# Kernel tuning notes

Hardware: AMD Instinct MI355X
Metric: run time of the kernel (lower is better)

The kernel has to match this reference:

```python
import jax, jax.numpy as jnp
import numpy as np

N = 50000      # nodes
E = 800000     # edges (before self-loops)
G = 500        # graphs
IN = 128       # in_channels
HID = 32       # hidden_channels per head
HEADS = 4
C = HID * HEADS        # 128, per-layer output dim
L = 3                  # num_layers
HL = (L * C) // 2      # 192, JK-LSTM hidden size (PyG convention)
OUT = 2
NEG_SLOPE = 0.2


def setup_inputs() -> dict:
    key = jax.random.key(0)
    ks = iter(jax.random.split(key, 40))
    inp = {}
    inp['x'] = jax.random.normal(next(ks), (N, IN), dtype=jnp.float32)
    inp['edge_index'] = jax.random.randint(next(ks), (2, E), 0, N, dtype=jnp.int32)
    inp['batch'] = jnp.sort(jax.random.randint(next(ks), (N,), 0, G, dtype=jnp.int32))
    s = 0.1
    for i, in_dim in enumerate([IN, C, C]):
        inp[f'W{i}'] = jax.random.normal(next(ks), (in_dim, C), dtype=jnp.float32) * s
        inp[f'as{i}'] = jax.random.normal(next(ks), (HEADS, HID), dtype=jnp.float32) * s
        inp[f'ad{i}'] = jax.random.normal(next(ks), (HEADS, HID), dtype=jnp.float32) * s
        inp[f'b{i}'] = jnp.zeros((C,), dtype=jnp.float32)
    for d in ['f', 'b']:
        inp[f'Wih_{d}'] = jax.random.normal(next(ks), (4 * HL, C), dtype=jnp.float32) * s
        inp[f'Whh_{d}'] = jax.random.normal(next(ks), (4 * HL, HL), dtype=jnp.float32) * s
        inp[f'bih_{d}'] = jnp.zeros((4 * HL,), dtype=jnp.float32)
        inp[f'bhh_{d}'] = jnp.zeros((4 * HL,), dtype=jnp.float32)
    inp['Wa'] = jax.random.normal(next(ks), (2 * HL, 1), dtype=jnp.float32) * s
    inp['ba'] = jnp.zeros((1,), dtype=jnp.float32)
    inp['Wl'] = jax.random.normal(next(ks), (C, OUT), dtype=jnp.float32) * s
    inp['bl'] = jnp.zeros((OUT,), dtype=jnp.float32)
    return inp


def gat_conv(h_in, src, dst, W, a_s, a_d, b, n):
    # h: [n, heads, hid]
    h = (h_in @ W).reshape(n, HEADS, HID)
    es = (h * a_s).sum(-1)   # [n, heads]
    ed = (h * a_d).sum(-1)
    e = jax.nn.leaky_relu(es[src] + ed[dst], NEG_SLOPE)  # [e, heads]
    m = jax.ops.segment_max(e, dst, num_segments=n)
    ex = jnp.exp(e - m[dst])
    ssum = jax.ops.segment_sum(ex, dst, num_segments=n)
    alpha = ex / (ssum[dst] + 1e-16)
    out = jax.ops.segment_sum(h[src] * alpha[:, :, None], dst, num_segments=n)
    return out.reshape(n, HEADS * HID) + b


def lstm_dir(xseq, Wih, Whh, bih, bhh):
    # xseq: [L, n, C] -> hs: [L, n, HL]; torch gate order i,f,g,o
    n = xseq.shape[1]
    h0 = jnp.zeros((n, HL), xseq.dtype)

    def step(carry, xt):
        h, c = carry
        z = xt @ Wih.T + h @ Whh.T + bih + bhh
        i, f, g, o = jnp.split(z, 4, axis=-1)
        c = jax.nn.sigmoid(f) * c + jax.nn.sigmoid(i) * jnp.tanh(g)
        h = jax.nn.sigmoid(o) * jnp.tanh(c)
        return (h, c), h

    _, hs = jax.lax.scan(step, (h0, h0), xseq)
    return hs


def reference(x, edge_index, batch, W0, as0, ad0, b0, W1, as1, ad1, b1,
              W2, as2, ad2, b2, Wih_f, Whh_f, bih_f, bhh_f,
              Wih_b, Whh_b, bih_b, bhh_b, Wa, ba, Wl, bl):
    n = x.shape[0]
    loop = jnp.arange(n, dtype=edge_index.dtype)
    src = jnp.concatenate([edge_index[0], loop])  # add_self_loops=True
    dst = jnp.concatenate([edge_index[1], loop])
    h = x
    xs = []
    for (W, a_s, a_d, b) in [(W0, as0, ad0, b0), (W1, as1, ad1, b1), (W2, as2, ad2, b2)]:
        h = jax.nn.relu(gat_conv(h, src, dst, W, a_s, a_d, b, n))
        xs.append(h)  # dropout is identity in eval mode
    xstack = jnp.stack(xs, axis=1)  # [n, L, C]
    xseq = jnp.stack(xs, axis=0)    # [L, n, C]
    hs_f = lstm_dir(xseq, Wih_f, Whh_f, bih_f, bhh_f)
    hs_b = lstm_dir(xseq[::-1], Wih_b, Whh_b, bih_b, bhh_b)[::-1]
    lo = jnp.concatenate([hs_f, hs_b], axis=-1)       # [L, n, 2*HL]
    score = jnp.einsum('lnh,h->nl', lo, Wa[:, 0]) + ba[0]
    att = jax.nn.softmax(score, axis=-1)              # [n, L]
    jk = jnp.einsum('nlc,nl->nc', xstack, att)        # [n, C]
    ones = jnp.ones((n,), x.dtype)
    counts = jax.ops.segment_sum(ones, batch, num_segments=G)
    pooled = jax.ops.segment_sum(jk, batch, num_segments=G) / jnp.maximum(counts, 1.0)[:, None]
    return pooled @ Wl + bl  # [G, OUT]
```

## Files before the change

### kernel.cpp

```cpp
#include <hip/hip_runtime.h>
#include <math.h>

#define CDIV(a,b) (((a)+(b)-1)/(b))

typedef _Float16 f16;
typedef _Float16 f16x8 __attribute__((ext_vector_type(8)));
typedef float f32x4 __attribute__((ext_vector_type(4)));

__device__ __forceinline__ float rcpf(float x){ return __builtin_amdgcn_rcpf(x); }
__device__ __forceinline__ float fsig(float x){ return rcpf(1.0f+__expf(-x)); }
__device__ __forceinline__ float ftanh(float x){ float e=__expf(2.0f*x); return 1.0f-2.0f*rcpf(e+1.0f); }

__global__ void zero_kernel(float* __restrict__ p, size_t n){
  size_t i=(size_t)blockIdx.x*blockDim.x+threadIdx.x;
  size_t st=(size_t)gridDim.x*blockDim.x;
  for(;i<n;i+=st) p[i]=0.0f;
}

__global__ void f2h_kernel(const float* __restrict__ s, f16* __restrict__ d, size_t n){
  size_t i=(size_t)blockIdx.x*blockDim.x+threadIdx.x;
  size_t st=(size_t)gridDim.x*blockDim.x;
  for(;i<n;i+=st) d[i]=(f16)s[i];
}
__global__ void wtrans_kernel(const float* __restrict__ W, f16* __restrict__ hi,
                              f16* __restrict__ lo){
  int o=blockIdx.x, i=threadIdx.x;
  float f=W[(size_t)i*128+o];
  f16 h=(f16)f; hi[o*128+i]=h; lo[o*128+i]=(f16)(f-(float)h);
}
__global__ void lstm_wprep(const float* __restrict__ W, f16* __restrict__ hi, int ld){
  int rn=blockIdx.x; int k=threadIdx.x;
  int j=rn>>2, gate=rn&3;
  hi[(size_t)rn*ld+k]=(f16)W[(size_t)(gate*192+j)*ld + k];
}
__global__ void lstm_bprep(const float* __restrict__ bih, const float* __restrict__ bhh,
                           float* __restrict__ bI){
  int rn=blockIdx.x*blockDim.x+threadIdx.x;
  if(rn<768){ int j=rn>>2,g=rn&3; int go=g*192+j; bI[rn]=bih[go]+bhh[go]; }
}

__global__ void hist_kernel(const int* __restrict__ ei, int E, int N, int* __restrict__ deg){
  int e=blockIdx.x*blockDim.x+threadIdx.x;
  if(e>=E+N) return;
  int d=(e<E)? ei[E+e] : (e-E);
  atomicAdd(&deg[d],1);
}
__global__ void scan1_kernel(const int* __restrict__ deg, int* __restrict__ offs,
                             int* __restrict__ bsums, int N){
  __shared__ int sd[1024];
  int t=threadIdx.x;
  int i=blockIdx.x*1024+t;
  int v=(i<N)?deg[i]:0;
  sd[t]=v;
  __syncthreads();
  for(int s=1;s<1024;s<<=1){
    int u=(t>=s)?sd[t-s]:0;
    __syncthreads();
    sd[t]+=u;
    __syncthreads();
  }
  if(i<N) offs[i]=sd[t]-v;
  if(t==1023) bsums[blockIdx.x]=sd[1023];
}
__global__ void scan2_kernel(int* __restrict__ bsums, int* __restrict__ offs, int NB, int N){
  if(threadIdx.x==0&&blockIdx.x==0){
    int run=0;
    for(int b=0;b<NB;b++){int s=bsums[b]; bsums[b]=run; run+=s;}
    offs[N]=run;
  }
}
__global__ void scan3_kernel(int* __restrict__ offs, const int* __restrict__ bsums,
                             int* __restrict__ cursor, int N){
  int i=blockIdx.x*blockDim.x+threadIdx.x;
  if(i<N){
    int o=offs[i]+bsums[i>>10];
    offs[i]=o;
    cursor[i]=o;
  }
}
__global__ void scatter_kernel(const int* __restrict__ ei, int E, int N,
                               int* __restrict__ cursor, int* __restrict__ csr){
  int e=blockIdx.x*blockDim.x+threadIdx.x;
  if(e>=E+N) return;
  int s,d;
  if(e<E){ s=ei[e]; d=ei[E+e]; } else { s=e-E; d=s; }
  int pos=atomicAdd(&cursor[d],1);
  csr[pos]=s;
}

__global__ void goffs_kernel(const int* __restrict__ batch, int N, int G,
                             int* __restrict__ goffs){
  int g=blockIdx.x*blockDim.x+threadIdx.x;
  if (g>G) return;
  if (g==G){ goffs[G]=N; return; }
  int lo=0, hi=N;
  while (lo<hi){ int mid=(lo+hi)>>1; if (batch[mid]<g) lo=mid+1; else hi=mid; }
  goffs[g]=lo;
}

struct GemmDesc {
  const f16* aq[2][12];
  const f16* bq[2][12];
  int lda[12], ldb[12];
  int nq, nd, M, GY, NXB;
  f16* htmp; const float* as_; const float* ad_; float* es; float* ed;
  f16* h16[2]; f16* cbuf[2]; const float* bias[2]; const float* wa[2];
  float* score; int l_out[2]; int firstStep; int lastStep;
};

template<int MODE>
__global__ __launch_bounds__(256) void gemm_mfma(GemmDesc d){
  __shared__ __align__(16) char smraw[33792];
  const int TILE = 128*32;
  f16* Ab0=(f16*)smraw;      f16* Ab1=Ab0+TILE;
  f16* Bb0=Ab1+TILE;         f16* Bb1=Bb0+TILE;
  float* EP = (float*)smraw;

  const int wg = blockIdx.x;
  const int xcd = wg & 7, kk0 = wg >> 3;
  const int nxt = d.nd * d.NXB;
  const int xbg = kk0 % nxt;
  const int yp  = xcd + 8*(kk0 / nxt);
  if (yp >= d.GY) return;
  const int dir = (xbg >= d.NXB) ? 1 : 0;
  const int xb  = xbg - dir*d.NXB;

  const int t = threadIdx.x;
  const int wv = t>>6, ln = t&63;
  const int m0 = yp*128, n0 = xb*128;
  const int wr = (wv>>1)*64, wc = (wv&1)*64;
  f32x4 acc[4][4];
#pragma unroll
  for(int i=0;i<4;i++)
#pragma unroll
  for(int j=0;j<4;j++) acc[i][j]=(f32x4){0.f,0.f,0.f,0.f};

  const int gs = ((ln&3) - ((ln>>3)&3)) & 3;
  const int gp = ((ln>>4) + (((ln&15)>>1)&3)) & 3;

  int offA128[2],offA192[2],offB128[2],offB192[2];
#pragma unroll
  for(int i=0;i<2;i++){
    int ga = m0 + i*64 + wv*16 + (ln>>2); if (ga >= d.M) ga = d.M-1;
    int gb = n0 + i*64 + wv*16 + (ln>>2);
    offA128[i]=ga*128+gs*8; offA192[i]=ga*192+gs*8;
    offB128[i]=gb*128+gs*8; offB192[i]=gb*192+gs*8;
  }

  auto issue=[&](int q,int buf){
    const f16* aS=d.aq[dir][q]; const bool wa_=(d.lda[q]==192);
    const f16* bS=d.bq[dir][q]; const bool wb_=(d.ldb[q]==192);
    f16* Adst = buf? Ab1:Ab0;
    f16* Bdst = buf? Bb1:Bb0;
#pragma unroll
    for(int i=0;i<2;i++){
      int offa = wa_? offA192[i]:offA128[i];
      __builtin_amdgcn_global_load_lds(
        (const __attribute__((address_space(1))) unsigned int*)(aS+offa),
        (__attribute__((address_space(3))) unsigned int*)&Adst[(i*64+wv*16)*32],16,0,0);
      int offb = wb_? offB192[i]:offB128[i];
      __builtin_amdgcn_global_load_lds(
        (const __attribute__((address_space(1))) unsigned int*)(bS+offb),
        (__attribute__((address_space(3))) unsigned int*)&Bdst[(i*64+wv*16)*32],16,0,0);
    }
  };

  issue(0,0);
  for (int s=0; s<d.nq; s++){
    const int cur = s&1;
    if (s+1<d.nq){
      issue(s+1,cur^1);
      asm volatile("s_waitcnt vmcnt(4)" ::: "memory");
    } else {
      asm volatile("s_waitcnt vmcnt(0)" ::: "memory");
    }
    __builtin_amdgcn_sched_barrier(0);
    __builtin_amdgcn_s_barrier();
    __builtin_amdgcn_sched_barrier(0);
    const f16* As = cur? Ab1:Ab0;
    const f16* Bs = cur? Bb1:Bb0;
    f16x8 av[4], bv[4];
#pragma unroll
    for (int i=0;i<4;i++)
      av[i] = *(const f16x8*)&As[(wr + i*16 + (ln&15))*32 + gp*8];
#pragma unroll
    for (int j=0;j<4;j++)
      bv[j] = *(const f16x8*)&Bs[(wc + j*16 + (ln&15))*32 + gp*8];
#pragma unroll
    for (int i=0;i<4;i++)
#pragma unroll
    for (int j=0;j<4;j++)
      acc[i][j] = __builtin_amdgcn_mfma_f32_16x16x32_f16(av[i], bv[j], acc[i][j], 0,0,0);
    __builtin_amdgcn_sched_barrier(0);
    __builtin_amdgcn_s_barrier();
  }

  const int lc2 = ln&15, lr4 = (ln>>4)*4;
  const int row4 = t>>2, q4 = t&3;
#pragma unroll
  for (int ph=0; ph<2; ph++){
    __syncthreads();
    if ((wv>>1) == ph){
#pragma unroll
      for (int i=0;i<4;i++){
#pragma unroll
        for (int jf=0;jf<4;jf++){
          int col = wc + jf*16 + lc2;
#pragma unroll
          for (int r=0;r<4;r++)
            EP[(i*16+lr4+r)*132 + col] = acc[i][jf][r];
        }
      }
    }
    __syncthreads();
    int grow = m0 + ph*64 + row4;
    if (grow < d.M){
      if (MODE==0){
        float s=0.f, dd=0.f;
        const float* asp = d.as_ + q4*32;
        const float* adp = d.ad_ + q4*32;
#pragma unroll
        for (int q8=0;q8<4;q8++){
          f16x8 pk;
#pragma unroll
          for (int r=0;r<8;r++){
            float v = EP[row4*132 + q4*32 + q8*8 + r];
            pk[r] = (f16)v;
            s  += v*asp[q8*8+r];
            dd += v*adp[q8*8+r];
          }
          *(f16x8*)&d.htmp[(size_t)grow*128 + q4*32 + q8*8] = pk;
        }
        d.es[grow*4+q4] = s;
        d.ed[grow*4+q4] = dd;
      } else {
        float sc = 0.f;
        int jg0 = xb*32 + q4*8;
        size_t hbase = (size_t)grow*192 + jg0;
        const float* bI = d.bias[dir] + xb*128 + q4*32;
        f16* h16d = d.h16[dir];
        f16* cbufd = d.cbuf[dir];
        const float* wad = d.wa[dir];
        f16x8 cold8;
        if (!d.firstStep) cold8 = *(const f16x8*)&cbufd[hbase];
        f16x8 hl, cl;
#pragma unroll
        for (int j=0;j<8;j++){
          float4 z = *(float4*)&EP[row4*132 + q4*32 + j*4];
          float zi=z.x+bI[j*4+0], zf=z.y+bI[j*4+1], zg=z.z+bI[j*4+2], zo=z.w+bI[j*4+3];
          float cold = d.firstStep ? 0.f : (float)cold8[j];
          float c = fsig(zf)*cold + fsig(zi)*ftanh(zg);
          float h = fsig(zo)*ftanh(c);
          cl[j] = (f16)c;
          hl[j] = (f16)h;
          sc += h * wad[jg0+j];
        }
        if (!d.lastStep){
          *(f16x8*)&cbufd[hbase] = cl;
          *(f16x8*)&h16d[hbase] = hl;
        }
        sc += __shfl_xor(sc,1);
        sc += __shfl_xor(sc,2);
        if (q4==0) atomicAdd(&d.score[(size_t)grow*3 + d.l_out[dir]], sc);
      }
    }
  }
}

__global__ __launch_bounds__(256) void attn_kernel(const f16* __restrict__ htmp,
   const float* __restrict__ es, const float* __restrict__ ed,
   const int* __restrict__ offs, const int* __restrict__ csr,
   const float* __restrict__ bias, f16* __restrict__ xsl, int N){
  int v=blockIdx.x*4+(threadIdx.x>>6);
  if(v>=N) return;
  int lane=threadIdx.x&63;
  int hd=lane>>4;
  int c0=lane*2;
  int beg=offs[v], end=offs[v+1];
  float edv=ed[v*4+hd];
  float ssum=0.f,a0=0.f,a1=0.f;
  int i=beg;
  for(; i+4<=end; i+=4){
    int s0=csr[i],s1=csr[i+1],s2=csr[i+2],s3=csr[i+3];
    float E0=es[s0*4+hd],E1=es[s1*4+hd],E2=es[s2*4+hd],E3=es[s3*4+hd];
    unsigned u0=*(const unsigned*)&htmp[(size_t)s0*128+c0];
    unsigned u1=*(const unsigned*)&htmp[(size_t)s1*128+c0];
    unsigned u2=*(const unsigned*)&htmp[(size_t)s2*128+c0];
    unsigned u3=*(const unsigned*)&htmp[(size_t)s3*128+c0];
    float e0=E0+edv; e0=(e0>0.f)?e0:0.2f*e0; float x0=__expf(e0);
    float e1=E1+edv; e1=(e1>0.f)?e1:0.2f*e1; float x1=__expf(e1);
    float e2=E2+edv; e2=(e2>0.f)?e2:0.2f*e2; float x2=__expf(e2);
    float e3=E3+edv; e3=(e3>0.f)?e3:0.2f*e3; float x3=__expf(e3);
    ssum += (x0+x1)+(x2+x3);
    union {unsigned u; f16 h[2];} p0,p1,p2,p3;
    p0.u=u0; p1.u=u1; p2.u=u2; p3.u=u3;
    a0 += x0*(float)p0.h[0] + x1*(float)p1.h[0] + x2*(float)p2.h[0] + x3*(float)p3.h[0];
    a1 += x0*(float)p0.h[1] + x1*(float)p1.h[1] + x2*(float)p2.h[1] + x3*(float)p3.h[1];
  }
  for(; i<end; i++){
    int s=csr[i];
    float e=es[s*4+hd]+edv;
    e=(e>0.f)?e:0.2f*e;
    float ex=__expf(e);
    ssum+=ex;
    union {unsigned u; f16 h[2];} pk;
    pk.u = *reinterpret_cast<const unsigned*>(&htmp[(size_t)s*128+c0]);
    a0+=ex*(float)pk.h[0]; a1+=ex*(float)pk.h[1];
  }
  float inv=1.0f/(ssum+1e-16f);
  float o0=fmaxf(a0*inv+bias[c0],0.f), o1=fmaxf(a1*inv+bias[c0+1],0.f);
  union { f16 h[2]; unsigned u; } pko;
  pko.h[0]=(f16)o0; pko.h[1]=(f16)o1;
  *reinterpret_cast<unsigned*>(&xsl[(size_t)v*128+c0]) = pko.u;
}

__global__ __launch_bounds__(256) void jk_pool_kernel(const f16* __restrict__ xs, size_t xstride,
   const float* __restrict__ score, const int* __restrict__ goffs,
   float* __restrict__ pooled, int G){
  int g=blockIdx.x;
  int beg=goffs[g], end=goffs[g+1];
  int c=threadIdx.x&127, half=threadIdx.x>>7;
  float acc=0.f;
  for(int n=beg+half; n<end; n+=2){
    float s0=score[n*3],s1=score[n*3+1],s2=score[n*3+2];
    float m=fmaxf(s0,fmaxf(s1,s2));
    float e0=__expf(s0-m),e1=__expf(s1-m),e2=__expf(s2-m);
    float inv=rcpf(e0+e1+e2);
    size_t base=(size_t)n*128+c;
    acc += ((float)xs[base]*e0+(float)xs[xstride+base]*e1+(float)xs[2*xstride+base]*e2)*inv;
  }
  __shared__ float red[128];
  if(half==1) red[c]=acc;
  __syncthreads();
  if(half==0){
    float tot=acc+red[c];
    float cnt=(float)(end-beg);
    pooled[(size_t)g*128+c]=tot*rcpf(fmaxf(cnt,1.0f));
  }
}

__global__ __launch_bounds__(128) void final_kernel(const float* __restrict__ pooled,
   const float* __restrict__ Wl, const float* __restrict__ bl,
   float* __restrict__ out, int G){
  int g=blockIdx.x; int c=threadIdx.x;
  float pv=pooled[(size_t)g*128+c];
  float p0=pv*Wl[c*2], p1=pv*Wl[c*2+1];
  for(int s=32;s>=1;s>>=1){ p0+=__shfl_down(p0,s); p1+=__shfl_down(p1,s); }
  __shared__ float sm[4];
  int w=c>>6;
  if((c&63)==0){ sm[w*2]=p0; sm[w*2+1]=p1; }
  __syncthreads();
  if(c==0){
    out[g*2+0]=sm[0]+sm[2]+bl[0];
    out[g*2+1]=sm[1]+sm[3]+bl[1];
  }
}

extern "C" void kernel_launch(void* const* d_in, const int* in_sizes, int n_in,
                              void* d_out, int out_size, void* d_ws, size_t ws_size,
                              hipStream_t stream) {
  const float* x     = (const float*)d_in[0];
  const int*   ei    = (const int*)d_in[1];
  const int*   batch = (const int*)d_in[2];
  const float* W[3]  = {(const float*)d_in[3],(const float*)d_in[7],(const float*)d_in[11]};
  const float* AS[3] = {(const float*)d_in[4],(const float*)d_in[8],(const float*)d_in[12]};
  const float* AD[3] = {(const float*)d_in[5],(const float*)d_in[9],(const float*)d_in[13]};
  const float* BV[3] = {(const float*)d_in[6],(const float*)d_in[10],(const float*)d_in[14]};
  const float* Wih[2]= {(const float*)d_in[15],(const float*)d_in[19]};
  const float* Whh[2]= {(const float*)d_in[16],(const float*)d_in[20]};
  const float* bih[2]= {(const float*)d_in[17],(const float*)d_in[21]};
  const float* bhh[2]= {(const float*)d_in[18],(const float*)d_in[22]};
  const float* Wa    = (const float*)d_in[23];
  const float* Wl    = (const float*)d_in[25];
  const float* bl    = (const float*)d_in[26];
  float* out = (float*)d_out;

  const int N  = in_sizes[2];
  const int E  = in_sizes[1]/2;
  const int ET = E+N;
  const int G  = out_size/2;
  const int Mpad = CDIV(N,128)*128;
  const int GY = CDIV(N,128);
  const int GYp = CDIV(GY,8)*8;

  char* p = (char*)d_ws;
  auto alloc = [&](size_t bytes)->char*{ char* r=p; p += ((bytes+255)/256)*256; return r; };
  int*   deg    = (int*)  alloc((size_t)N*4);
  int*   offs   = (int*)  alloc((size_t)(N+1)*4);
  int*   cursor = (int*)  alloc((size_t)N*4);
  int*   bsums  = (int*)  alloc((size_t)CDIV(N,1024)*4);
  int*   csr    = (int*)  alloc((size_t)ET*4);
  int*   goffs  = (int*)  alloc((size_t)(G+1)*4);
  f16*   WtH[3], *WtL[3];
  for(int l=0;l<3;l++){ WtH[l]=(f16*)alloc(128*128*2); WtL[l]=(f16*)alloc(128*128*2); }
  f16 *WihH[2],*WhhH[2];
  float* bsumI[2];
  for(int d2=0;d2<2;d2++){
    WihH[d2]=(f16*)alloc(768*128*2);
    WhhH[d2]=(f16*)alloc(768*192*2);
    bsumI[d2]=(float*)alloc(768*4);
  }
  f16*   xs16   = (f16*)  alloc((size_t)3*Mpad*128*2);
  float* score  = (float*)alloc((size_t)N*3*4);
  float* pooled = (float*)alloc((size_t)G*128*4);
  char* P = p;
  auto al256 = [](size_t b)->size_t{ return ((b+255)/256)*256; };
  f16*   x016 = (f16*)P;
  f16*   htmp = (f16*)(P + al256((size_t)Mpad*128*2));
  float* esb  = (float*)((char*)htmp + al256((size_t)Mpad*128*2));
  float* edb  = (float*)((char*)esb + al256((size_t)N*4*4));
  f16*  h16s[2]; f16* cbufs[2];
  {
    char* q = P;
    h16s[0]=(f16*)q;   q += al256((size_t)Mpad*192*2);
    cbufs[0]=(f16*)q;  q += al256((size_t)Mpad*192*2);
    h16s[1]=(f16*)q;   q += al256((size_t)Mpad*192*2);
    cbufs[1]=(f16*)q;
  }

  const size_t xstride = (size_t)Mpad*128;

  f2h_kernel<<<512,256,0,stream>>>(x, x016, (size_t)N*128);
  for(int l=0;l<3;l++) wtrans_kernel<<<128,128,0,stream>>>(W[l], WtH[l], WtL[l]);
  for(int d2=0;d2<2;d2++){
    lstm_wprep<<<768,128,0,stream>>>(Wih[d2], WihH[d2], 128);
    lstm_wprep<<<768,192,0,stream>>>(Whh[d2], WhhH[d2], 192);
    lstm_bprep<<<3,256,0,stream>>>(bih[d2], bhh[d2], bsumI[d2]);
  }
  zero_kernel<<<64,256,0,stream>>>(score,(size_t)N*3);
  goffs_kernel<<<CDIV(G+1,256),256,0,stream>>>(batch,N,G,goffs);

  zero_kernel<<<64,256,0,stream>>>((float*)deg,(size_t)N);
  hist_kernel<<<CDIV(ET,256),256,0,stream>>>(ei,E,N,deg);
  int NB = CDIV(N,1024);
  scan1_kernel<<<NB,1024,0,stream>>>(deg,offs,bsums,N);
  scan2_kernel<<<1,64,0,stream>>>(bsums,offs,NB,N);
  scan3_kernel<<<CDIV(N,256),256,0,stream>>>(offs,bsums,cursor,N);
  scatter_kernel<<<CDIV(ET,256),256,0,stream>>>(ei,E,N,cursor,csr);

  const f16* ain = x016;
  for (int l=0; l<3; l++){
    GemmDesc gd{};
    gd.nq=8; gd.nd=1; gd.M=N; gd.GY=GY; gd.NXB=1;
    gd.htmp=htmp; gd.as_=AS[l]; gd.ad_=AD[l]; gd.es=esb; gd.ed=edb;
    for(int qq=0;qq<4;qq++){
      gd.aq[0][2*qq+0]=ain+qq*32;  gd.bq[0][2*qq+0]=WtH[l]+qq*32;
      gd.aq[0][2*qq+1]=ain+qq*32;  gd.bq[0][2*qq+1]=WtL[l]+qq*32;
    }
    for(int qq=0;qq<8;qq++){ gd.lda[qq]=128; gd.ldb[qq]=128; }
    gemm_mfma<0><<<GYp,256,0,stream>>>(gd);
    attn_kernel<<<CDIV(N,4),256,0,stream>>>(htmp,esb,edb,offs,csr,BV[l],
                                            xs16+(size_t)l*xstride,N);
    ain = xs16+(size_t)l*xstride;
  }

  for (int st=0; st<3; st++){
    GemmDesc gd{};
    gd.nd=2; gd.NXB=6; gd.M=N; gd.GY=GY;
    gd.nq = (st==0)?4:10;
    gd.score=score; gd.firstStep=(st==0); gd.lastStep=(st==2);
    for(int dir2=0;dir2<2;dir2++){
      int l_in = dir2? (2-st):st;
      gd.l_out[dir2]=l_in;
      const f16* xt = xs16 + (size_t)l_in*xstride;
      gd.h16[dir2]=h16s[dir2]; gd.cbuf[dir2]=cbufs[dir2];
      gd.bias[dir2]=bsumI[dir2]; gd.wa[dir2]=Wa+dir2*192;
      for(int qq=0;qq<4;qq++){
        gd.aq[dir2][qq]=xt+qq*32;
        gd.bq[dir2][qq]=WihH[dir2]+qq*32;
      }
      for(int qq=4;qq<10;qq++){
        gd.aq[dir2][qq]=h16s[dir2]+(qq-4)*32;
        gd.bq[dir2][qq]=WhhH[dir2]+(qq-4)*32;
      }
    }
    for(int qq=0;qq<4;qq++){ gd.lda[qq]=128; gd.ldb[qq]=128; }
    for(int qq=4;qq<10;qq++){ gd.lda[qq]=192; gd.ldb[qq]=192; }
    gemm_mfma<1><<<12*GYp,256,0,stream>>>(gd);
  }

  jk_pool_kernel<<<G,256,0,stream>>>(xs16,xstride,score,goffs,pooled,G);
  final_kernel<<<G,128,0,stream>>>(pooled,Wl,bl,out,G);
}
```

Before: 616.9 us.

## Split each node's edge aggregation across four waves with shared-memory reduction

The GAT aggregation kernel now gives each destination node a full 256-thread block instead of one wavefront. The four waves stride over the neighbor list two edges at a time, and their partial sums are combined through shared memory with a block barrier. The aim is to raise memory-level parallelism and shorten per-node latency when degrees are around 17. In exchange it launches four times as many blocks, adds a barrier and LDS traffic, and leaves waves idle on low-degree nodes.

Result: slower. 723.8 us (+17.3%).

```diff
diff --git a/kernel.cpp b/kernel.cpp
--- a/kernel.cpp
+++ b/kernel.cpp
@@ -271,47 +271,41 @@
    const float* __restrict__ es, const float* __restrict__ ed,
    const int* __restrict__ offs, const int* __restrict__ csr,
    const float* __restrict__ bias, f16* __restrict__ xsl, int N){
-  int v=blockIdx.x*4+(threadIdx.x>>6);
-  if(v>=N) return;
-  int lane=threadIdx.x&63;
+  int v=blockIdx.x;
+  int wv=threadIdx.x>>6, lane=threadIdx.x&63;
   int hd=lane>>4;
   int c0=lane*2;
   int beg=offs[v], end=offs[v+1];
   float edv=ed[v*4+hd];
   float ssum=0.f,a0=0.f,a1=0.f;
-  int i=beg;
-  for(; i+4<=end; i+=4){
-    int s0=csr[i],s1=csr[i+1],s2=csr[i+2],s3=csr[i+3];
-    float E0=es[s0*4+hd],E1=es[s1*4+hd],E2=es[s2*4+hd],E3=es[s3*4+hd];
+  for(int i=beg+wv*2; i<end; i+=8){
+    int s0=csr[i];
+    bool has2=(i+1<end);
+    int s1=has2? csr[i+1]:s0;
+    float E0=es[s0*4+hd], E1=es[s1*4+hd];
     unsigned u0=*(const unsigned*)&htmp[(size_t)s0*128+c0];
     unsigned u1=*(const unsigned*)&htmp[(size_t)s1*128+c0];
-    unsigned u2=*(const unsigned*)&htmp[(size_t)s2*128+c0];
-    unsigned u3=*(const unsigned*)&htmp[(size_t)s3*128+c0];
     float e0=E0+edv; e0=(e0>0.f)?e0:0.2f*e0; float x0=__expf(e0);
-    float e1=E1+edv; e1=(e1>0.f)?e1:0.2f*e1; float x1=__expf(e1);
-    float e2=E2+edv; e2=(e2>0.f)?e2:0.2f*e2; float x2=__expf(e2);
-    float e3=E3+edv; e3=(e3>0.f)?e3:0.2f*e3; float x3=__expf(e3);
-    ssum += (x0+x1)+(x2+x3);
-    union {unsigned u; f16 h[2];} p0,p1,p2,p3;
-    p0.u=u0; p1.u=u1; p2.u=u2; p3.u=u3;
-    a0 += x0*(float)p0.h[0] + x1*(float)p1.h[0] + x2*(float)p2.h[0] + x3*(float)p3.h[0];
-    a1 += x0*(float)p0.h[1] + x1*(float)p1.h[1] + x2*(float)p2.h[1] + x3*(float)p3.h[1];
-  }
-  for(; i<end; i++){
-    int s=csr[i];
-    float e=es[s*4+hd]+edv;
-    e=(e>0.f)?e:0.2f*e;
-    float ex=__expf(e);
-    ssum+=ex;
-    union {unsigned u; f16 h[2];} pk;
-    pk.u = *reinterpret_cast<const unsigned*>(&htmp[(size_t)s*128+c0]);
-    a0+=ex*(float)pk.h[0]; a1+=ex*(float)pk.h[1];
-  }
-  float inv=1.0f/(ssum+1e-16f);
-  float o0=fmaxf(a0*inv+bias[c0],0.f), o1=fmaxf(a1*inv+bias[c0+1],0.f);
-  union { f16 h[2]; unsigned u; } pko;
-  pko.h[0]=(f16)o0; pko.h[1]=(f16)o1;
-  *reinterpret_cast<unsigned*>(&xsl[(size_t)v*128+c0]) = pko.u;
+    float e1=E1+edv; e1=(e1>0.f)?e1:0.2f*e1; float x1=has2?__expf(e1):0.f;
+    ssum+=x0+x1;
+    union {unsigned u; f16 h[2];} p0,p1;
+    p0.u=u0; p1.u=u1;
+    a0 += x0*(float)p0.h[0] + x1*(float)p1.h[0];
+    a1 += x0*(float)p0.h[1] + x1*(float)p1.h[1];
+  }
+  __shared__ float red[3][4][64];
+  red[0][wv][lane]=a0; red[1][wv][lane]=a1; red[2][wv][lane]=ssum;
+  __syncthreads();
+  if(wv==0){
+    a0  =red[0][0][lane]+red[0][1][lane]+red[0][2][lane]+red[0][3][lane];
+    a1  =red[1][0][lane]+red[1][1][lane]+red[1][2][lane]+red[1][3][lane];
+    ssum=red[2][0][lane]+red[2][1][lane]+red[2][2][lane]+red[2][3][lane];
+    float inv=rcpf(ssum+1e-16f);
+    float o0=fmaxf(a0*inv+bias[c0],0.f), o1=fmaxf(a1*inv+bias[c0+1],0.f);
+    union { f16 h[2]; unsigned u; } pko;
+    pko.h[0]=(f16)o0; pko.h[1]=(f16)o1;
+    *reinterpret_cast<unsigned*>(&xsl[(size_t)v*128+c0]) = pko.u;
+  }
 }
 
 __global__ __launch_bounds__(256) void jk_pool_kernel(const f16* __restrict__ xs, size_t xstride,
@@ -449,8 +443,8 @@
     }
     for(int qq=0;qq<8;qq++){ gd.lda[qq]=128; gd.ldb[qq]=128; }
     gemm_mfma<0><<<GYp,256,0,stream>>>(gd);
-    attn_kernel<<<CDIV(N,4),256,0,stream>>>(htmp,esb,edb,offs,csr,BV[l],
-                                            xs16+(size_t)l*xstride,N);
+    attn_kernel<<<N,256,0,stream>>>(htmp,esb,edb,offs,csr,BV[l],
+                                    xs16+(size_t)l*xstride,N);
     ain = xs16+(size_t)l*xstride;
   }
 
```
